# Kernel optimization log

Hardware: AMD Instinct MI355X
Metric: run time of the kernel (lower is better)

## Reference

```python
import jax, jax.numpy as jnp
import numpy as np

B, T, I, H, O = 64, 512, 128, 1024, 128
ALPHA = 0.2


def setup_inputs() -> dict:
    key = jax.random.key(0)
    ks = jax.random.split(key, 7)
    inv_sqrt_h = 1.0 / np.sqrt(H)
    return {
        "x": jax.random.normal(ks[0], (B, T, I), dtype=jnp.float32),
        "wi": jax.random.normal(ks[1], (I, H), dtype=jnp.float32) / np.sqrt(I),
        "wrec": jax.random.normal(ks[2], (H, H), dtype=jnp.float32) * inv_sqrt_h,
        "wout": jax.random.normal(ks[3], (H, O), dtype=jnp.float32) * inv_sqrt_h,
        "b": jax.random.normal(ks[4], (H, 1), dtype=jnp.float32) * 0.1,
        "g": jax.random.normal(ks[5], (H, 1), dtype=jnp.float32) * 0.5 + 1.0,
        "h0": jax.random.normal(ks[6], (H,), dtype=jnp.float32) * 0.1,
    }


def reference(x, wi, wrec, wout, b, g, h0):
    # Leaky tanh RNN: h_{t+1} = h_t + alpha*(-h_t + (g*r_t) @ wrec^T + x_t @ wi)
    #                 r_t = tanh(h_t + b); out_t = (g*r_t) @ wout
    gv = g[:, 0]  # (H,)
    bv = b[:, 0]  # (H,)
    batch = x.shape[0]

    r0 = jnp.tanh(h0 + bv)                     # (H,)
    out0 = (gv * r0) @ wout                    # (O,) broadcast over batch

    h_init = jnp.broadcast_to(h0, (batch, h0.shape[0]))
    r_init = jnp.broadcast_to(r0, (batch, h0.shape[0]))

    # precompute input projection for all steps used in the loop (steps 0..T-2)
    xs = jnp.swapaxes(x[:, :-1, :], 0, 1)      # (T-1, B, I)

    def step(carry, x_t):
        h, r = carry
        h = h + ALPHA * (-h + (gv * r) @ wrec.T + x_t @ wi)
        r = jnp.tanh(h + bv)
        out = (gv * r) @ wout                  # (B, O)
        return (h, r), out

    _, outs = jax.lax.scan(step, (h_init, r_init), xs)   # (T-1, B, O)
    outs = jnp.swapaxes(outs, 0, 1)                      # (B, T-1, O)
    out0b = jnp.broadcast_to(out0, (batch, 1, wout.shape[1]))
    return jnp.concatenate([out0b, outs], axis=1)        # (B, T, O)
```

## Files before the change

kernel.cpp:

```cpp
#include <hip/hip_runtime.h>

#define H 1024
#define I_DIM 128
#define O_DIM 128
#define T_DIM 512
#define ALPHA 0.2f
#define NWG 64
#define GSZ 16
#define PLANE_U64 2048
#define GRP_U64   (3 * PLANE_U64)

typedef short short8 __attribute__((ext_vector_type(8)));
typedef float f32x4 __attribute__((ext_vector_type(4)));
typedef unsigned long long ull_alias __attribute__((may_alias));

__device__ __forceinline__ unsigned short f2b(float f) {
    union { float f; unsigned u; } x; x.f = f;
    unsigned u = x.u;
    return (unsigned short)((u + 0x7FFFu + ((u >> 16) & 1u)) >> 16);
}
__device__ __forceinline__ float tanh_fast(float x) {
    float e = __expf(2.0f * x);
    return 1.0f - 2.0f * __builtin_amdgcn_rcpf(e + 1.0f);
}
__device__ __forceinline__ short8 ld8f(const float* __restrict__ p) {
    const float4 a = *(const float4*)p;
    const float4 b = *(const float4*)(p + 4);
    short8 r;
    r[0]=(short)f2b(a.x); r[1]=(short)f2b(a.y); r[2]=(short)f2b(a.z); r[3]=(short)f2b(a.w);
    r[4]=(short)f2b(b.x); r[5]=(short)f2b(b.y); r[6]=(short)f2b(b.z); r[7]=(short)f2b(b.w);
    return r;
}
__device__ __forceinline__ short8 pack8(float4 a, float4 b) {
    short8 r;
    r[0]=(short)f2b(a.x); r[1]=(short)f2b(a.y); r[2]=(short)f2b(a.z); r[3]=(short)f2b(a.w);
    r[4]=(short)f2b(b.x); r[5]=(short)f2b(b.y); r[6]=(short)f2b(b.z); r[7]=(short)f2b(b.w);
    return r;
}

__global__ __launch_bounds__(256, 1) void rnn_kernel(
    const float* __restrict__ x, const float* __restrict__ wi,
    const float* __restrict__ wrec, const float* __restrict__ wout,
    const float* __restrict__ bb, const float* __restrict__ gg,
    const float* __restrict__ h0p, float* __restrict__ out,
    unsigned long long* __restrict__ aG)
{
    __shared__ unsigned short abuf[32 * 512];
    __shared__ unsigned short aloc[1024];
    __shared__ float opart[4 * 128];

    const int tid  = threadIdx.x;
    const int w    = tid >> 6, lane = tid & 63;
    const int n    = lane & 15, q = lane >> 4;
    const int grp  = blockIdx.x & 3;
    const int ji   = blockIdx.x >> 2;
    const int j0   = ji * 64;
    const int j    = j0 + w * 16 + n;
    const int b0   = grp * 16;

    short8 wfr[32];
#pragma unroll
    for (int kt = 0; kt < 32; ++kt)
        wfr[kt] = ld8f(&wrec[(size_t)j * H + kt * 32 + q * 8]);

    short8 wifr[4];
#pragma unroll
    for (int kt = 0; kt < 4; ++kt) {
        short8 v;
#pragma unroll
        for (int i = 0; i < 8; ++i)
            v[i] = (short)f2b(wi[(size_t)(kt * 32 + q * 8 + i) * H + j]);
        wifr[kt] = v;
    }
    short8 wofr[8];
#pragma unroll
    for (int kk = 0; kk < 8; ++kk) {
        short8 v;
        const int kb = (w * 8 + kk) * 32 + q * 8;
#pragma unroll
        for (int i = 0; i < 8; ++i)
            v[i] = (n < 8) ? (short)f2b(wout[(size_t)(kb + i) * O_DIM + ji * 8 + n]) : (short)0;
        wofr[kk] = v;
    }

    const float gv = gg[j], bv = bb[j], h00 = h0p[j];
    float hreg[4];
#pragma unroll
    for (int r = 0; r < 4; ++r) hreg[r] = h00;

    const int kl    = w * 16 + n;
    const int off_l = (kl >> 5) * 512 + ((kl & 31) >> 3) * 128 + (kl & 7);
    const int s_sl  = ji * 4 + w;

    unsigned long long* const gB0 = aG + grp * GRP_U64;
    unsigned long long* const gB1 = aG + (4 + grp) * GRP_U64;

    const int pubA = (lane >> 5) * PLANE_U64 + s_sl * 32 + (lane & 31);
    const int pubB = 2 * PLANE_U64 + s_sl * 32 + lane;
    const int oA   = lane & 31;

    const int cbase = w * 512 + lane;

    int doff[8];
#pragma unroll
    for (int i = 0; i < 8; ++i) {
        const int idx = i * 64 + lane;
        const int s   = 16 * w + (idx >> 5);
        const int oo  = idx & 31;
        const int m   = oo >> 1, so = oo & 1;
        const int k0  = (s >> 2) * 64 + (s & 3) * 16 + so * 8;
        doff[i] = ((k0 >> 5) * 512 + ((k0 & 31) >> 3) * 128 + m * 8) * 2;
    }

    auto publish = [&](int t) {
        asm volatile("" ::: "memory");
        const unsigned long long tagv = (unsigned long long)(unsigned)t << 48;
        unsigned long long* gb = (t & 1) ? gB1 : gB0;
        {
            const ull_alias* opq = (const ull_alias*)&aloc[w * 256 + (oA & 1) * 128 + (oA >> 1) * 8];
            const unsigned long long lo = opq[0], hi = opq[1];
            const unsigned long long d0 = lo & 0x0000FFFFFFFFFFFFull;
            const unsigned long long d1 = ((lo >> 48) | (hi << 16)) & 0x0000FFFFFFFFFFFFull;
            __hip_atomic_store(gb + pubA, ((lane < 32) ? d0 : d1) | tagv,
                               __ATOMIC_RELAXED, __HIP_MEMORY_SCOPE_AGENT);
        }
        if (lane < 32) {
            const ull_alias* opq = (const ull_alias*)&aloc[w * 256 + (lane & 1) * 128 + (lane >> 1) * 8];
            const unsigned long long hi = opq[1];
            const unsigned long long d2 = ((hi >> 32) & 0xFFFFFFFFull) | tagv;
            __hip_atomic_store(gb + pubB, d2, __ATOMIC_RELAXED, __HIP_MEMORY_SCOPE_AGENT);
        }
    };

    auto consume = [&](int tv) {
        const unsigned tt = (unsigned)tv;
        const unsigned long long* gb = (tv & 1) ? gB1 : gB0;
        unsigned long long v0[8], v1[8], v2[8];
        for (;;) {
#pragma unroll
            for (int i = 0; i < 8; ++i) {
                v0[i] = __hip_atomic_load(gb + cbase + i * 64,
                                          __ATOMIC_RELAXED, __HIP_MEMORY_SCOPE_AGENT);
                v1[i] = __hip_atomic_load(gb + PLANE_U64 + cbase + i * 64,
                                          __ATOMIC_RELAXED, __HIP_MEMORY_SCOPE_AGENT);
                v2[i] = __hip_atomic_load(gb + 2 * PLANE_U64 + cbase + i * 64,
                                          __ATOMIC_RELAXED, __HIP_MEMORY_SCOPE_AGENT);
            }
            unsigned bad = 0;
#pragma unroll
            for (int i = 0; i < 8; ++i)
                bad |= ((unsigned)(v0[i] >> 48) ^ tt) | ((unsigned)(v1[i] >> 48) ^ tt)
                     | ((unsigned)(v2[i] >> 48) ^ tt);
            if (__all(bad == 0)) break;
            __builtin_amdgcn_s_sleep(1);
        }
        asm volatile("" ::: "memory");
#pragma unroll
        for (int i = 0; i < 8; ++i) {
            const unsigned long long ca = v0[i], cb = v1[i], cc = v2[i];
            const unsigned long long w01 = (ca & 0xFFFFFFFFull)
                | (((ca >> 32) & 0xFFFFull) << 32) | ((cb & 0xFFFFull) << 48);
            const unsigned long long w23 = ((cb >> 16) & 0xFFFFFFFFull) | (cc << 32);
            ull_alias* d = (ull_alias*)((char*)abuf + doff[i]);
            d[0] = w01; d[1] = w23;
        }
    };

    auto do_out = [&](int t) {
        f32x4 oa = {0.f, 0.f, 0.f, 0.f};
#pragma unroll
        for (int kk = 0; kk < 8; ++kk) {
            short8 af = *(const short8*)&abuf[(w * 8 + kk) * 512 + lane * 8];
            oa = __builtin_amdgcn_mfma_f32_16x16x32_bf16(af, wofr[kk], oa, 0, 0, 0);
        }
        if (n < 8) {
#pragma unroll
            for (int r = 0; r < 4; ++r) opart[w * 128 + (4 * q + r) * 8 + n] = oa[r];
        }
        __syncthreads();
        if (tid < 128) {
            float s = opart[tid] + opart[128 + tid] + opart[256 + tid] + opart[384 + tid];
            const int m = tid >> 3, c = tid & 7;
            out[((size_t)(b0 + m) * T_DIM + t) * O_DIM + ji * 8 + c] = s;
        }
    };

    {
        unsigned short a0 = f2b(gv * tanh_fast(h00 + bv));
#pragma unroll
        for (int r = 0; r < 4; ++r) aloc[off_l + (4 * q + r) * 8] = a0;
        publish(0);
    }

    short8 xfr[4];
#pragma unroll
    for (int kt = 0; kt < 4; ++kt)
        xfr[kt] = ld8f(&x[(size_t)(b0 + n) * T_DIM * I_DIM + kt * 32 + q * 8]);

    float4 xr[8];

    for (int t = 1; t < T_DIM; ++t) {
        if (t < T_DIM - 1) {
            const float* xp = &x[((size_t)(b0 + n) * T_DIM + t) * I_DIM];
#pragma unroll
            for (int kt = 0; kt < 4; ++kt) {
                xr[2 * kt]     = *(const float4*)(xp + kt * 32 + q * 8);
                xr[2 * kt + 1] = *(const float4*)(xp + kt * 32 + q * 8 + 4);
            }
        }

        f32x4 acc0 = {0.f,0.f,0.f,0.f}, acc1 = {0.f,0.f,0.f,0.f};
        acc0 = __builtin_amdgcn_mfma_f32_16x16x32_bf16(xfr[0], wifr[0], acc0, 0,0,0);
        acc1 = __builtin_amdgcn_mfma_f32_16x16x32_bf16(xfr[1], wifr[1], acc1, 0,0,0);
        acc0 = __builtin_amdgcn_mfma_f32_16x16x32_bf16(xfr[2], wifr[2], acc0, 0,0,0);
        acc1 = __builtin_amdgcn_mfma_f32_16x16x32_bf16(xfr[3], wifr[3], acc1, 0,0,0);

        __syncthreads();
        consume(t - 1);
        __syncthreads();

#pragma unroll
        for (int kt = 0; kt < 32; kt += 2) {
            short8 a0f = *(const short8*)&abuf[kt * 512 + lane * 8];
            short8 a1f = *(const short8*)&abuf[(kt + 1) * 512 + lane * 8];
            acc0 = __builtin_amdgcn_mfma_f32_16x16x32_bf16(a0f, wfr[kt],     acc0, 0,0,0);
            acc1 = __builtin_amdgcn_mfma_f32_16x16x32_bf16(a1f, wfr[kt + 1], acc1, 0,0,0);
        }

#pragma unroll
        for (int r = 0; r < 4; ++r) {
            float z  = acc0[r] + acc1[r];
            float hv = (1.0f - ALPHA) * hreg[r] + ALPHA * z;
            hreg[r] = hv;
            aloc[off_l + (4 * q + r) * 8] = f2b(gv * tanh_fast(hv + bv));
        }
        publish(t);

        if (t < T_DIM - 1) {
#pragma unroll
            for (int kt = 0; kt < 4; ++kt)
                xfr[kt] = pack8(xr[2 * kt], xr[2 * kt + 1]);
        }
        do_out(t - 1);
    }

    __syncthreads();
    consume(T_DIM - 1);
    __syncthreads();
    do_out(T_DIM - 1);
}

extern "C" void kernel_launch(void* const* d_in, const int* in_sizes, int n_in,
                              void* d_out, int out_size, void* d_ws, size_t ws_size,
                              hipStream_t stream) {
    const float* x    = (const float*)d_in[0];
    const float* wi   = (const float*)d_in[1];
    const float* wrec = (const float*)d_in[2];
    const float* wout = (const float*)d_in[3];
    const float* bb   = (const float*)d_in[4];
    const float* gg   = (const float*)d_in[5];
    const float* h0   = (const float*)d_in[6];
    float* outp = (float*)d_out;

    unsigned long long* aG = (unsigned long long*)d_ws;

    hipMemsetAsync(d_ws, 0xFF, (size_t)2 * 4 * GRP_U64 * 8, stream);
    hipLaunchKernelGGL(rnn_kernel, dim3(NWG), dim3(256), 0, stream,
                       x, wi, wrec, wout, bb, gg, h0, outp, aG);
}
```

Measured before the change: 1.847 ms.

## Issue cross-workgroup state polls early and simplify unpack addressing via lane permutation

The first round of atomic loads that poll the previous step's published state now starts at the top of each timestep, before the x loads and input-projection MFMAs. The tag check and any retry loop run after the barrier, so the global-memory latency of the first poll can overlap that work. The per-lane scatter offsets (doff) are replaced by a permuted read index, which lets unpack write contiguous 16-byte chunks into LDS. The risk is that the early poll often sees stale tags and forces an extra round-trip, and the permutation changes which data each lane reads.

```diff
diff --git a/kernel.cpp b/kernel.cpp
--- a/kernel.cpp
+++ b/kernel.cpp
@@ -99,18 +99,8 @@
     const int pubB = 2 * PLANE_U64 + s_sl * 32 + lane;
     const int oA   = lane & 31;
 
-    const int cbase = w * 512 + lane;
-
-    int doff[8];
-#pragma unroll
-    for (int i = 0; i < 8; ++i) {
-        const int idx = i * 64 + lane;
-        const int s   = 16 * w + (idx >> 5);
-        const int oo  = idx & 31;
-        const int m   = oo >> 1, so = oo & 1;
-        const int k0  = (s >> 2) * 64 + (s & 3) * 16 + so * 8;
-        doff[i] = ((k0 >> 5) * 512 + ((k0 & 31) >> 3) * 128 + m * 8) * 2;
-    }
+    const int perm  = (lane >> 5) * 32 + (lane & 15) * 2 + ((lane >> 4) & 1);
+    const int cb    = w * 512 + perm;
 
     auto publish = [&](int t) {
         asm volatile("" ::: "memory");
@@ -132,20 +122,25 @@
         }
     };
 
-    auto consume = [&](int tv) {
+    auto poll_issue = [&](const unsigned long long* gb,
+                          unsigned long long* v0, unsigned long long* v1,
+                          unsigned long long* v2) {
+#pragma unroll
+        for (int i = 0; i < 8; ++i) {
+            v0[i] = __hip_atomic_load(gb + cb + i * 64,
+                                      __ATOMIC_RELAXED, __HIP_MEMORY_SCOPE_AGENT);
+            v1[i] = __hip_atomic_load(gb + PLANE_U64 + cb + i * 64,
+                                      __ATOMIC_RELAXED, __HIP_MEMORY_SCOPE_AGENT);
+            v2[i] = __hip_atomic_load(gb + 2 * PLANE_U64 + cb + i * 64,
+                                      __ATOMIC_RELAXED, __HIP_MEMORY_SCOPE_AGENT);
+        }
+    };
+
+    auto poll_check = [&](int tv, const unsigned long long* gb,
+                          unsigned long long* v0, unsigned long long* v1,
+                          unsigned long long* v2) {
         const unsigned tt = (unsigned)tv;
-        const unsigned long long* gb = (tv & 1) ? gB1 : gB0;
-        unsigned long long v0[8], v1[8], v2[8];
         for (;;) {
-#pragma unroll
-            for (int i = 0; i < 8; ++i) {
-                v0[i] = __hip_atomic_load(gb + cbase + i * 64,
-                                          __ATOMIC_RELAXED, __HIP_MEMORY_SCOPE_AGENT);
-                v1[i] = __hip_atomic_load(gb + PLANE_U64 + cbase + i * 64,
-                                          __ATOMIC_RELAXED, __HIP_MEMORY_SCOPE_AGENT);
-                v2[i] = __hip_atomic_load(gb + 2 * PLANE_U64 + cbase + i * 64,
-                                          __ATOMIC_RELAXED, __HIP_MEMORY_SCOPE_AGENT);
-            }
             unsigned bad = 0;
 #pragma unroll
             for (int i = 0; i < 8; ++i)
@@ -153,15 +148,20 @@
                      | ((unsigned)(v2[i] >> 48) ^ tt);
             if (__all(bad == 0)) break;
             __builtin_amdgcn_s_sleep(1);
+            poll_issue(gb, v0, v1, v2);
         }
         asm volatile("" ::: "memory");
+    };
+
+    auto unpack = [&](const unsigned long long* v0, const unsigned long long* v1,
+                      const unsigned long long* v2) {
 #pragma unroll
         for (int i = 0; i < 8; ++i) {
-            const unsigned long long ca = v0[i], cb = v1[i], cc = v2[i];
+            const unsigned long long ca = v0[i], cb_ = v1[i], cc = v2[i];
             const unsigned long long w01 = (ca & 0xFFFFFFFFull)
-                | (((ca >> 32) & 0xFFFFull) << 32) | ((cb & 0xFFFFull) << 48);
-            const unsigned long long w23 = ((cb >> 16) & 0xFFFFFFFFull) | (cc << 32);
-            ull_alias* d = (ull_alias*)((char*)abuf + doff[i]);
+                | (((ca >> 32) & 0xFFFFull) << 32) | ((cb_ & 0xFFFFull) << 48);
+            const unsigned long long w23 = ((cb_ >> 16) & 0xFFFFFFFFull) | (cc << 32);
+            ull_alias* d = (ull_alias*)((char*)abuf + w * 8192 + (i * 64 + lane) * 16);
             d[0] = w01; d[1] = w23;
         }
     };
@@ -198,8 +198,13 @@
         xfr[kt] = ld8f(&x[(size_t)(b0 + n) * T_DIM * I_DIM + kt * 32 + q * 8]);
 
     float4 xr[8];
+    unsigned long long pv0[8], pv1[8], pv2[8];
 
     for (int t = 1; t < T_DIM; ++t) {
+        const unsigned long long* gb = ((t - 1) & 1) ? gB1 : gB0;
+
+        poll_issue(gb, pv0, pv1, pv2);
+
         if (t < T_DIM - 1) {
             const float* xp = &x[((size_t)(b0 + n) * T_DIM + t) * I_DIM];
 #pragma unroll
@@ -216,7 +221,8 @@
         acc1 = __builtin_amdgcn_mfma_f32_16x16x32_bf16(xfr[3], wifr[3], acc1, 0,0,0);
 
         __syncthreads();
-        consume(t - 1);
+        poll_check(t - 1, gb, pv0, pv1, pv2);
+        unpack(pv0, pv1, pv2);
         __syncthreads();
 
 #pragma unroll
@@ -244,10 +250,15 @@
         do_out(t - 1);
     }
 
-    __syncthreads();
-    consume(T_DIM - 1);
-    __syncthreads();
-    do_out(T_DIM - 1);
+    {
+        const unsigned long long* gb = ((T_DIM - 1) & 1) ? gB1 : gB0;
+        poll_issue(gb, pv0, pv1, pv2);
+        __syncthreads();
+        poll_check(T_DIM - 1, gb, pv0, pv1, pv2);
+        unpack(pv0, pv1, pv2);
+        __syncthreads();
+        do_out(T_DIM - 1);
+    }
 }
 
 extern "C" void kernel_launch(void* const* d_in, const int* in_sizes, int n_in,
```

Result: faster. 1.789 ms (-3.1%).
